# Optimization experiments

Measured on AMD Instinct MI355X. Metric: run time of the kernel, lower is better.

## Reference

```python
import jax, jax.numpy as jnp
import numpy as np

E = 768   # embed_size
H = 64    # head_embed_size
B = 8
T = 4096  # == ctx_size


def setup_inputs() -> dict:
    key = jax.random.key(0)
    k1, k2, k3, k4 = jax.random.split(key, 4)
    inputs = jax.random.normal(k1, (B, T, E), dtype=jnp.float32)
    # Linear weights stored as (E, H) so projection is x @ W
    scale = 1.0 / np.sqrt(E)
    Wq = jax.random.uniform(k2, (E, H), dtype=jnp.float32, minval=-scale, maxval=scale)
    Wk = jax.random.uniform(k3, (E, H), dtype=jnp.float32, minval=-scale, maxval=scale)
    Wv = jax.random.uniform(k4, (E, H), dtype=jnp.float32, minval=-scale, maxval=scale)
    return {"inputs": inputs, "Wq": Wq, "Wk": Wk, "Wv": Wv}


def reference(inputs, Wq, Wk, Wv):
    Tlen = inputs.shape[1]
    q = inputs @ Wq  # (B,T,H)
    k = inputs @ Wk  # (B,T,H)
    v = inputs @ Wv  # (B,T,H)
    # NOTE: original module does NOT scale by 1/sqrt(H) — faithful reproduction.
    scores = jnp.einsum('bqh,bkh->bqk', q, k)  # (B,T,T)
    causal = jnp.tril(jnp.ones((Tlen, Tlen), dtype=bool))
    scores = jnp.where(causal, scores, -jnp.inf)
    attn = jax.nn.softmax(scores, axis=-1)
    # dropout=0 -> identity
    out = jnp.einsum('bqk,bkh->bqh', attn, v)  # (B,T,H)
    return out
```

## Files before the change

### kernel.cpp

```cpp
#include <hip/hip_runtime.h>
#include <hip/hip_bf16.h>

#define E_DIM 768
#define H_DIM 64
#define B_SZ 8
#define T_SZ 4096
#define BT (B_SZ * T_SZ)

typedef __attribute__((ext_vector_type(8))) short short8;
typedef __attribute__((ext_vector_type(4))) float floatx4;

#define RAWBAR() __asm__ volatile("s_waitcnt lgkmcnt(0)\n\ts_barrier" ::: "memory")

static __device__ __forceinline__ unsigned short bf1(float a) {
    __hip_bfloat16 h = __float2bfloat16(a);
    unsigned short u; __builtin_memcpy(&u, &h, 2); return u;
}
static __device__ __forceinline__ unsigned int pk2(float a, float b) {
    __hip_bfloat162 h = __float22bfloat162_rn(float2{a, b});
    unsigned int u; __builtin_memcpy(&u, &h, 4); return u;
}

__global__ __launch_bounds__(256) void prep_w(
    const float* __restrict__ Wq, const float* __restrict__ Wk,
    const float* __restrict__ Wv, unsigned short* __restrict__ Wt)
{
    __shared__ float Ls[64][65];
    const int nt = blockIdx.x;
    const int kc = blockIdx.y;
    const float* __restrict__ W = (nt == 0) ? Wq : (nt == 1) ? Wk : Wv;
    const float scl = (nt == 0) ? 1.44269504088896f : 1.0f;
    const int t = threadIdx.x;
    const int k0 = kc * 64;

#pragma unroll
    for (int it = 0; it < 16; ++it) {
        const int kk = (t >> 6) + it * 4;
        Ls[kk][t & 63] = W[(size_t)(k0 + kk) * H_DIM + (t & 63)];
    }
    __syncthreads();

#pragma unroll
    for (int it = 0; it < 4; ++it) {
        const int nl = (t >> 4) + it * 16;
        const int kl = (t & 15) * 4;
        unsigned int u[2];
        u[0] = pk2(Ls[kl + 0][nl] * scl, Ls[kl + 1][nl] * scl);
        u[1] = pk2(Ls[kl + 2][nl] * scl, Ls[kl + 3][nl] * scl);
        *(uint2*)(Wt + (size_t)(nt * 64 + nl) * E_DIM + k0 + kl) = *(uint2*)u;
    }
}

__global__ __launch_bounds__(768) void proj_mfma(
    const float* __restrict__ X, const unsigned short* __restrict__ Wt,
    unsigned short* __restrict__ Qb, unsigned short* __restrict__ Kb,
    unsigned short* __restrict__ Vtb)
{
    __shared__ unsigned short Xs[2][16][776];

    const int tid  = threadIdx.x;
    const int wave = tid >> 6, lane = tid & 63;
    const int row  = lane & 15, quad = lane >> 4;
    const int m0   = blockIdx.x * 128;

    short8 bfr[24];
    {
        const unsigned short* wp = Wt + (size_t)(wave * 16 + row) * E_DIM + quad * 8;
#pragma unroll
        for (int ks = 0; ks < 24; ++ks) bfr[ks] = *(const short8*)(wp + ks * 32);
    }

    const int srow = tid & 15;
    const int sc   = tid >> 4;
    const float* __restrict__ xbase = X + (size_t)(m0 + srow) * E_DIM + sc * 16;

    float4 fx[4];
#define LDX(mt)                                                               \
    {                                                                         \
        const float* p = xbase + (size_t)(mt) * 16 * E_DIM;                   \
        fx[0] = *(const float4*)(p);     fx[1] = *(const float4*)(p + 4);     \
        fx[2] = *(const float4*)(p + 8); fx[3] = *(const float4*)(p + 12);    \
    }
#define STX(buf)                                                              \
    {                                                                         \
        unsigned int tmp[8];                                                  \
        tmp[0] = pk2(fx[0].x, fx[0].y); tmp[1] = pk2(fx[0].z, fx[0].w);       \
        tmp[2] = pk2(fx[1].x, fx[1].y); tmp[3] = pk2(fx[1].z, fx[1].w);       \
        tmp[4] = pk2(fx[2].x, fx[2].y); tmp[5] = pk2(fx[2].z, fx[2].w);       \
        tmp[6] = pk2(fx[3].x, fx[3].y); tmp[7] = pk2(fx[3].z, fx[3].w);       \
        *(int4*)&Xs[buf][srow][sc * 16]     = *(int4*)&tmp[0];                \
        *(int4*)&Xs[buf][srow][sc * 16 + 8] = *(int4*)&tmp[4];                \
    }

    LDX(0); STX(0);
    RAWBAR();

    const int g  = wave >> 2;
    const int h  = (wave & 3) * 16 + row;
    unsigned short* __restrict__ OQK = (g == 0) ? Qb : Kb;
    const int bb = m0 >> 12;

    int cur = 0;
    for (int mt = 0; mt < 8; ++mt) {
        if (mt < 7) LDX(mt + 1);

        floatx4 acc = (floatx4)0.0f;
#pragma unroll
        for (int ks = 0; ks < 24; ++ks) {
            const short8 af = *(const short8*)&Xs[cur][row][ks * 32 + quad * 8];
            acc = __builtin_amdgcn_mfma_f32_16x16x32_bf16(af, bfr[ks], acc, 0, 0, 0);
        }

        const int mr = m0 + mt * 16 + quad * 4;
        if (g < 2) {
#pragma unroll
            for (int r = 0; r < 4; ++r)
                OQK[(size_t)(mr + r) * H_DIM + h] = bf1(acc[r]);
        } else {
            const int t0 = mr & 4095;
            unsigned int u[2];
            u[0] = pk2(acc[0], acc[1]); u[1] = pk2(acc[2], acc[3]);
            *(uint2*)(Vtb + ((size_t)bb * H_DIM + h) * T_SZ + t0) = *(uint2*)u;
        }

        if (mt < 7) STX(cur ^ 1);
        RAWBAR();
        cur ^= 1;
    }
#undef LDX
#undef STX
}

__global__ __launch_bounds__(256, 4) void attn_mfma(
    const unsigned short* __restrict__ Qb,
    const unsigned short* __restrict__ Kb,
    const unsigned short* __restrict__ Vtb,
    float* __restrict__ Out)
{
    __shared__ __align__(16) unsigned short KV[2][64][72];
    __shared__ __align__(16) unsigned short Ps[4][16][40];
    __shared__ float lc[4][16];

    const int lb   = blockIdx.x;
    const int b    = lb & 7;
    const int qq   = 127 - (lb >> 3);
    const int tid  = threadIdx.x;
    const int wave = tid >> 6, lane = tid & 63;
    const int col  = lane & 15, quad = lane >> 4;
    const int wq   = wave >> 1;
    const int wk   = wave & 1;

    const size_t base = (size_t)b * T_SZ * H_DIM;
    const int q0  = qq * 32;
    const int nkt = (qq >> 1) + 1;
    const int ktd = nkt - 1;

    short8 qf0, qf1;
    {
        const unsigned short* qp = Qb + base + (size_t)(q0 + wq * 16 + col) * H_DIM + quad * 8;
        qf0 = *(const short8*)(qp);
        qf1 = *(const short8*)(qp + 32);
    }

    floatx4 o[4];
#pragma unroll
    for (int i = 0; i < 4; ++i) o[i] = (floatx4)0.0f;
    float lp[4] = {0.0f, 0.0f, 0.0f, 0.0f};

    const int krow = tid >> 2, kcol = (tid & 3) * 16;
    const unsigned short* __restrict__ Ksrc = Kb + base + (size_t)krow * H_DIM + kcol;
    const unsigned short* __restrict__ Vsrc = Vtb + ((size_t)b * H_DIM + krow) * T_SZ + kcol;

    int4 kr0, kr1, vr0, vr1;
#define LDKV(t)                                                          \
    {                                                                    \
        const unsigned short* kp = Ksrc + (size_t)(t) * 64 * H_DIM;      \
        kr0 = *(const int4*)kp; kr1 = *(const int4*)(kp + 8);            \
        const unsigned short* vp = Vsrc + (t) * 64;                      \
        vr0 = *(const int4*)vp; vr1 = *(const int4*)(vp + 8);            \
    }
#define STKV()                                                           \
    {                                                                    \
        *(int4*)&KV[0][krow][kcol] = kr0; *(int4*)&KV[0][krow][kcol + 8] = kr1; \
        *(int4*)&KV[1][krow][kcol] = vr0; *(int4*)&KV[1][krow][kcol + 8] = vr1; \
    }

    LDKV(0);
    STKV();
    RAWBAR();

    for (int kt = 0; kt < nkt; ++kt) {
        if (kt + 1 < nkt) LDKV(kt + 1);

        floatx4 s[2];
#pragma unroll
        for (int j = 0; j < 2; ++j) {
            const unsigned short* kp = &KV[0][(wk * 2 + j) * 16 + col][quad * 8];
            floatx4 a = (floatx4)0.0f;
            a = __builtin_amdgcn_mfma_f32_16x16x32_bf16(qf0, *(const short8*)(kp),      a, 0, 0, 0);
            a = __builtin_amdgcn_mfma_f32_16x16x32_bf16(qf1, *(const short8*)(kp + 32), a, 0, 0, 0);
            s[j] = a;
        }

        if (kt == ktd) {
#pragma unroll
            for (int j = 0; j < 2; ++j) {
                const int keyg = kt * 64 + wk * 32 + j * 16 + col;
#pragma unroll
                for (int r = 0; r < 4; ++r)
                    if (keyg > q0 + wq * 16 + quad * 4 + r) s[j][r] = -1e30f;
            }
        }

#pragma unroll
        for (int r = 0; r < 4; ++r) {
#pragma unroll
            for (int j = 0; j < 2; ++j) {
                const float pv = exp2f(fminf(s[j][r], 110.0f));
                lp[r] += pv;
                Ps[wave][quad * 4 + r][j * 16 + col] = bf1(pv);
            }
        }
        __builtin_amdgcn_wave_barrier();

        {
            const short8 pa = *(const short8*)(&Ps[wave][col][quad * 8]);
#pragma unroll
            for (int d = 0; d < 4; ++d) {
                const short8 vb = *(const short8*)(&KV[1][d * 16 + col][wk * 32 + quad * 8]);
                o[d] = __builtin_amdgcn_mfma_f32_16x16x32_bf16(pa, vb, o[d], 0, 0, 0);
            }
        }

        RAWBAR();
        if (kt + 1 < nkt) STKV();
        RAWBAR();
    }

#pragma unroll
    for (int r = 0; r < 4; ++r) {
        float l = lp[r];
#pragma unroll
        for (int off = 1; off < 16; off <<= 1)
            l += __shfl_xor(l, off, 16);
        if (col == 0) lc[wave][quad * 4 + r] = l;
    }
    __syncthreads();

    float* __restrict__ Oc = (float*)&KV[0][0][0];
#pragma unroll
    for (int r = 0; r < 4; ++r)
#pragma unroll
        for (int d = 0; d < 4; ++d)
            Oc[((wave * 16) + quad * 4 + r) * 64 + d * 16 + col] = o[d][r];
    __syncthreads();

    {
        const int orow = tid >> 3;
        const int d0   = (tid & 7) * 8;
        const int rl   = orow & 15;
        const int wb   = (orow >> 4) * 2;
        const float* p0 = &Oc[((wb * 16) + rl) * 64 + d0];
        const float* p1 = &Oc[(((wb + 1) * 16) + rl) * 64 + d0];
        const float inv = 1.0f / (lc[wb][rl] + lc[wb + 1][rl]);
        float4 a0 = *(const float4*)(p0);
        float4 a1 = *(const float4*)(p0 + 4);
        const float4 b0 = *(const float4*)(p1);
        const float4 b1 = *(const float4*)(p1 + 4);
        a0.x = (a0.x + b0.x) * inv; a0.y = (a0.y + b0.y) * inv;
        a0.z = (a0.z + b0.z) * inv; a0.w = (a0.w + b0.w) * inv;
        a1.x = (a1.x + b1.x) * inv; a1.y = (a1.y + b1.y) * inv;
        a1.z = (a1.z + b1.z) * inv; a1.w = (a1.w + b1.w) * inv;
        float* op = Out + base + (size_t)(q0 + orow) * H_DIM + d0;
        *(float4*)(op)     = a0;
        *(float4*)(op + 4) = a1;
    }
#undef LDKV
#undef STKV
}

extern "C" void kernel_launch(void* const* d_in, const int* in_sizes, int n_in,
                              void* d_out, int out_size, void* d_ws, size_t ws_size,
                              hipStream_t stream) {
    const float* X  = (const float*)d_in[0];
    const float* Wq = (const float*)d_in[1];
    const float* Wk = (const float*)d_in[2];
    const float* Wv = (const float*)d_in[3];

    unsigned short* Wt  = (unsigned short*)d_ws;
    unsigned short* Qb  = Wt + (size_t)192 * E_DIM;
    unsigned short* Kb  = Qb + (size_t)BT * H_DIM;
    unsigned short* Vtb = Kb + (size_t)BT * H_DIM;

    prep_w<<<dim3(3, 12), 256, 0, stream>>>(Wq, Wk, Wv, Wt);
    proj_mfma<<<256, 768, 0, stream>>>(X, Wt, Qb, Kb, Vtb);
    attn_mfma<<<1024, 256, 0, stream>>>(Qb, Kb, Vtb, (float*)d_out);
}
```

Measured before the change: 230.8 us.

## Deepen prefetch pipelines in projection and attention kernels, drop exp clamp

```diff
diff --git a/kernel.cpp b/kernel.cpp
--- a/kernel.cpp
+++ b/kernel.cpp
@@ -51,12 +51,12 @@
     }
 }
 
-__global__ __launch_bounds__(768) void proj_mfma(
+__global__ __launch_bounds__(768, 3) void proj_mfma(
     const float* __restrict__ X, const unsigned short* __restrict__ Wt,
     unsigned short* __restrict__ Qb, unsigned short* __restrict__ Kb,
     unsigned short* __restrict__ Vtb)
 {
-    __shared__ unsigned short Xs[2][16][776];
+    __shared__ unsigned short Xs[3][16][776];
 
     const int tid  = threadIdx.x;
     const int wave = tid >> 6, lane = tid & 63;
@@ -70,29 +70,31 @@
         for (int ks = 0; ks < 24; ++ks) bfr[ks] = *(const short8*)(wp + ks * 32);
     }
 
-    const int srow = tid & 15;
-    const int sc   = tid >> 4;
+    const int srow = tid / 48;
+    const int sc   = tid % 48;
     const float* __restrict__ xbase = X + (size_t)(m0 + srow) * E_DIM + sc * 16;
 
-    float4 fx[4];
-#define LDX(mt)                                                               \
+    float4 fx[2][4];
+#define LDX(slot, mt)                                                         \
     {                                                                         \
         const float* p = xbase + (size_t)(mt) * 16 * E_DIM;                   \
-        fx[0] = *(const float4*)(p);     fx[1] = *(const float4*)(p + 4);     \
-        fx[2] = *(const float4*)(p + 8); fx[3] = *(const float4*)(p + 12);    \
-    }
-#define STX(buf)                                                              \
+        fx[slot][0] = *(const float4*)(p);     fx[slot][1] = *(const float4*)(p + 4);  \
+        fx[slot][2] = *(const float4*)(p + 8); fx[slot][3] = *(const float4*)(p + 12); \
+    }
+#define STX(slot, buf)                                                        \
     {                                                                         \
         unsigned int tmp[8];                                                  \
-        tmp[0] = pk2(fx[0].x, fx[0].y); tmp[1] = pk2(fx[0].z, fx[0].w);       \
-        tmp[2] = pk2(fx[1].x, fx[1].y); tmp[3] = pk2(fx[1].z, fx[1].w);       \
-        tmp[4] = pk2(fx[2].x, fx[2].y); tmp[5] = pk2(fx[2].z, fx[2].w);       \
-        tmp[6] = pk2(fx[3].x, fx[3].y); tmp[7] = pk2(fx[3].z, fx[3].w);       \
+        tmp[0] = pk2(fx[slot][0].x, fx[slot][0].y); tmp[1] = pk2(fx[slot][0].z, fx[slot][0].w); \
+        tmp[2] = pk2(fx[slot][1].x, fx[slot][1].y); tmp[3] = pk2(fx[slot][1].z, fx[slot][1].w); \
+        tmp[4] = pk2(fx[slot][2].x, fx[slot][2].y); tmp[5] = pk2(fx[slot][2].z, fx[slot][2].w); \
+        tmp[6] = pk2(fx[slot][3].x, fx[slot][3].y); tmp[7] = pk2(fx[slot][3].z, fx[slot][3].w); \
         *(int4*)&Xs[buf][srow][sc * 16]     = *(int4*)&tmp[0];                \
         *(int4*)&Xs[buf][srow][sc * 16 + 8] = *(int4*)&tmp[4];                \
     }
 
-    LDX(0); STX(0);
+    LDX(0, 0);
+    LDX(1, 1);
+    STX(0, 0);
     RAWBAR();
 
     const int g  = wave >> 2;
@@ -100,14 +102,19 @@
     unsigned short* __restrict__ OQK = (g == 0) ? Qb : Kb;
     const int bb = m0 >> 12;
 
-    int cur = 0;
+    int bcur = 0;
     for (int mt = 0; mt < 8; ++mt) {
-        if (mt < 7) LDX(mt + 1);
+        if (mt + 2 < 8) LDX(mt & 1, mt + 2);
+        if (mt + 1 < 8) {
+            int bnext = bcur + 1; if (bnext == 3) bnext = 0;
+            STX((mt + 1) & 1, bnext);
+        }
+        RAWBAR();
 
         floatx4 acc = (floatx4)0.0f;
 #pragma unroll
         for (int ks = 0; ks < 24; ++ks) {
-            const short8 af = *(const short8*)&Xs[cur][row][ks * 32 + quad * 8];
+            const short8 af = *(const short8*)&Xs[bcur][row][ks * 32 + quad * 8];
             acc = __builtin_amdgcn_mfma_f32_16x16x32_bf16(af, bfr[ks], acc, 0, 0, 0);
         }
 
@@ -123,9 +130,7 @@
             *(uint2*)(Vtb + ((size_t)bb * H_DIM + h) * T_SZ + t0) = *(uint2*)u;
         }
 
-        if (mt < 7) STX(cur ^ 1);
-        RAWBAR();
-        cur ^= 1;
+        ++bcur; if (bcur == 3) bcur = 0;
     }
 #undef LDX
 #undef STX
@@ -137,7 +142,7 @@
     const unsigned short* __restrict__ Vtb,
     float* __restrict__ Out)
 {
-    __shared__ __align__(16) unsigned short KV[2][64][72];
+    __shared__ __align__(16) unsigned short KV[2][2][64][72];
     __shared__ __align__(16) unsigned short Ps[4][16][40];
     __shared__ float lc[4][16];
 
@@ -171,31 +176,37 @@
     const unsigned short* __restrict__ Ksrc = Kb + base + (size_t)krow * H_DIM + kcol;
     const unsigned short* __restrict__ Vsrc = Vtb + ((size_t)b * H_DIM + krow) * T_SZ + kcol;
 
-    int4 kr0, kr1, vr0, vr1;
-#define LDKV(t)                                                          \
+    int4 kr[2][2], vr[2][2];
+#define LDKV(slot, t)                                                    \
     {                                                                    \
         const unsigned short* kp = Ksrc + (size_t)(t) * 64 * H_DIM;      \
-        kr0 = *(const int4*)kp; kr1 = *(const int4*)(kp + 8);            \
+        kr[slot][0] = *(const int4*)kp; kr[slot][1] = *(const int4*)(kp + 8); \
         const unsigned short* vp = Vsrc + (t) * 64;                      \
-        vr0 = *(const int4*)vp; vr1 = *(const int4*)(vp + 8);            \
-    }
-#define STKV()                                                           \
+        vr[slot][0] = *(const int4*)vp; vr[slot][1] = *(const int4*)(vp + 8); \
+    }
+#define STKV(slot, buf)                                                  \
     {                                                                    \
-        *(int4*)&KV[0][krow][kcol] = kr0; *(int4*)&KV[0][krow][kcol + 8] = kr1; \
-        *(int4*)&KV[1][krow][kcol] = vr0; *(int4*)&KV[1][krow][kcol + 8] = vr1; \
-    }
-
-    LDKV(0);
-    STKV();
+        *(int4*)&KV[buf][0][krow][kcol]     = kr[slot][0];               \
+        *(int4*)&KV[buf][0][krow][kcol + 8] = kr[slot][1];               \
+        *(int4*)&KV[buf][1][krow][kcol]     = vr[slot][0];               \
+        *(int4*)&KV[buf][1][krow][kcol + 8] = vr[slot][1];               \
+    }
+
+    LDKV(0, 0);
+    STKV(0, 0);
+    if (nkt > 1) LDKV(1, 1);
     RAWBAR();
 
     for (int kt = 0; kt < nkt; ++kt) {
-        if (kt + 1 < nkt) LDKV(kt + 1);
+        if (kt + 2 < nkt) LDKV(kt & 1, kt + 2);
+        if (kt + 1 < nkt) STKV((kt + 1) & 1, (kt + 1) & 1);
+
+        const int buf = kt & 1;
 
         floatx4 s[2];
 #pragma unroll
         for (int j = 0; j < 2; ++j) {
-            const unsigned short* kp = &KV[0][(wk * 2 + j) * 16 + col][quad * 8];
+            const unsigned short* kp = &KV[buf][0][(wk * 2 + j) * 16 + col][quad * 8];
             floatx4 a = (floatx4)0.0f;
             a = __builtin_amdgcn_mfma_f32_16x16x32_bf16(qf0, *(const short8*)(kp),      a, 0, 0, 0);
             a = __builtin_amdgcn_mfma_f32_16x16x32_bf16(qf1, *(const short8*)(kp + 32), a, 0, 0, 0);
@@ -216,7 +227,7 @@
         for (int r = 0; r < 4; ++r) {
 #pragma unroll
             for (int j = 0; j < 2; ++j) {
-                const float pv = exp2f(fminf(s[j][r], 110.0f));
+                const float pv = exp2f(s[j][r]);
                 lp[r] += pv;
                 Ps[wave][quad * 4 + r][j * 16 + col] = bf1(pv);
             }
@@ -227,13 +238,11 @@
             const short8 pa = *(const short8*)(&Ps[wave][col][quad * 8]);
 #pragma unroll
             for (int d = 0; d < 4; ++d) {
-                const short8 vb = *(const short8*)(&KV[1][d * 16 + col][wk * 32 + quad * 8]);
+                const short8 vb = *(const short8*)(&KV[buf][1][d * 16 + col][wk * 32 + quad * 8]);
                 o[d] = __builtin_amdgcn_mfma_f32_16x16x32_bf16(pa, vb, o[d], 0, 0, 0);
             }
         }
 
-        RAWBAR();
-        if (kt + 1 < nkt) STKV();
         RAWBAR();
     }
 
@@ -247,7 +256,7 @@
     }
     __syncthreads();
 
-    float* __restrict__ Oc = (float*)&KV[0][0][0];
+    float* __restrict__ Oc = (float*)&KV[0][0][0][0];
 #pragma unroll
     for (int r = 0; r < 4; ++r)
 #pragma unroll
```

Result: slower. 329.0 us (+42.5%).
